# Kernel optimization log

Measured on AMD Instinct MI355X. Metric: run time of the kernel, lower is better.

## Reference

```python
import jax, jax.numpy as jnp
import numpy as np

B, S, D, H = 4, 2048, 1024, 16
DH = D // H


def setup_inputs() -> dict:
    key = jax.random.key(0)
    ks = jax.random.split(key, 10)
    scale = 1.0 / np.sqrt(D)
    return {
        "query": jax.random.normal(ks[0], (B, S, D), dtype=jnp.float32),
        "mask": jax.random.randint(ks[1], (B, S, S), 0, 2).astype(jnp.bool_),
        "Wq": jax.random.normal(ks[2], (D, D), dtype=jnp.float32) * scale,
        "bq": jax.random.normal(ks[3], (D,), dtype=jnp.float32) * 0.01,
        "Wk": jax.random.normal(ks[4], (D, D), dtype=jnp.float32) * scale,
        "bk": jax.random.normal(ks[5], (D,), dtype=jnp.float32) * 0.01,
        "Wv": jax.random.normal(ks[6], (D, D), dtype=jnp.float32) * scale,
        "bv": jax.random.normal(ks[7], (D,), dtype=jnp.float32) * 0.01,
        "Wo": jax.random.normal(ks[8], (D, D), dtype=jnp.float32) * scale,
        "bo": jax.random.normal(ks[9], (D,), dtype=jnp.float32) * 0.01,
    }


def reference(query, mask, Wq, bq, Wk, bk, Wv, bv, Wo, bo):
    # Self-attention path (key=value=None): q,k,v all from `query`.
    # Linear layers use torch convention: x @ W.T + b.  [B,S,D]
    q = query @ Wq.T + bq
    k = query @ Wk.T + bk
    v = query @ Wv.T + bv

    # split heads: [B,S,D] -> [B,H,S,DH]
    def split(x):
        return x.reshape(B, S, H, DH).transpose(0, 2, 1, 3)

    q, k, v = split(q), split(k), split(v)

    # scaled dot-product scores: [B,H,Sq,Sk]
    scores = jnp.einsum("bhqd,bhkd->bhqk", q, k) / jnp.sqrt(
        jnp.asarray(DH, dtype=q.dtype)
    )
    # MULTIPLICATIVE mask (True where masked), broadcast over heads
    scores = scores * mask[:, None, :, :].astype(scores.dtype)

    attn = jax.nn.softmax(scores, axis=-1)  # [B,H,Sq,Sk]
    out = jnp.einsum("bhqk,bhkd->bhqd", attn, v)  # [B,H,Sq,DH]

    # merge heads: [B,H,S,DH] -> [B,S,D]
    out = out.transpose(0, 2, 1, 3).reshape(B, S, D)
    return out @ Wo.T + bo
```

## Files before the change

### kernel.cpp

```cpp
#include <hip/hip_runtime.h>
#include <hip/hip_bf16.h>

#define DEVINL __device__ __forceinline__

typedef __attribute__((ext_vector_type(8))) short bf16x8;
typedef __attribute__((ext_vector_type(4))) float f32x4;

static constexpr int Bb = 4, Ss = 2048, Dd = 1024, Hh = 16, DHh = 64;
#define QPRESCALE 0.18033688f

DEVINL unsigned short f2bf(float f) {
  union { float f; unsigned int u; } a; a.f = f;
  unsigned int u = a.u;
  return (unsigned short)((u + 0x7fffu + ((u >> 16) & 1u)) >> 16);
}

DEVINL unsigned short f2bf_rne(float f) {
  __hip_bfloat16 h = __float2bfloat16(f);
  return *reinterpret_cast<unsigned short*>(&h);
}

DEVINL float fexp2(float x) {
#if __has_builtin(__builtin_amdgcn_exp2f)
  return __builtin_amdgcn_exp2f(x);
#else
  float r; asm("v_exp_f32 %0, %1" : "=v"(r) : "v"(x)); return r;
#endif
}

DEVINL unsigned cvtpk_bf16(float lo, float hi) {
  unsigned r; asm("v_cvt_pk_bf16_f32 %0, %1, %2" : "=v"(r) : "v"(lo), "v"(hi));
  return r;
}

DEVINL void gload16(const void* g, void* l) {
  __builtin_amdgcn_global_load_lds((const __attribute__((address_space(1))) void*)g,
                                   (__attribute__((address_space(3))) void*)l, 16, 0, 0);
}

__global__ void cvt_f32_bf16(const float4* __restrict__ src, ushort* __restrict__ dst, int n4) {
  int i = blockIdx.x * blockDim.x + threadIdx.x;
  int stride = gridDim.x * blockDim.x;
  for (; i < n4; i += stride) {
    float4 v = src[i];
    ushort4 o;
    o.x = f2bf(v.x); o.y = f2bf(v.y); o.z = f2bf(v.z); o.w = f2bf(v.w);
    *reinterpret_cast<ushort4*>(dst + (size_t)i * 4) = o;
  }
}

__global__ void bias_cat(const float* __restrict__ bq, const float* __restrict__ bk,
                         const float* __restrict__ bv, float* __restrict__ bcat) {
  int i = blockIdx.x * blockDim.x + threadIdx.x;
  if (i < 1024) bcat[i] = bq[i];
  else if (i < 2048) bcat[i] = bk[i - 1024];
  else if (i < 3072) bcat[i] = bv[i - 2048];
}

__global__ void mask_bits(const int* __restrict__ mask, unsigned long long* __restrict__ bm) {
  const int tid = threadIdx.x, lane = tid & 63;
  const int gw = blockIdx.x * 4 + (tid >> 6);
  const int b = gw >> 16;
  const int rem = gw & 65535;
  const int s = rem >> 5, ch = rem & 31;
  int m = mask[((size_t)b * Ss + s) * Ss + ch * 64 + lane];
  unsigned long long bits = __ballot(m != 0);
  if (lane == 0) bm[((size_t)b * 32 + ch) * Ss + s] = bits;
}

template<int OUT_BF16, int QSCALE>
__global__ __launch_bounds__(256)
void gemm_bt(const ushort* __restrict__ A, const ushort* __restrict__ Bm,
             const float* __restrict__ bias, void* __restrict__ Cout,
             ushort* __restrict__ vT, int M, int N, int K, int ldc) {
  __shared__ short lA[128 * 32];
  __shared__ short lB[128 * 32];
  const int tid = threadIdx.x;
  const int lane = tid & 63;
  const int wid = tid >> 6;
  const int wm = wid >> 1, wn = wid & 1;
  const int row0 = blockIdx.x * 128, col0 = blockIdx.y * 128;
  const int lr = lane & 15, lk8 = (lane >> 4) * 8;

  f32x4 acc[4][4];
#pragma unroll
  for (int i = 0; i < 4; i++)
#pragma unroll
    for (int j = 0; j < 4; j++) acc[i][j] = (f32x4){0.f, 0.f, 0.f, 0.f};

  const int c0 = tid, c1 = tid + 256;
  const int r0s = c0 >> 2, k0s = c0 & 3;
  const int r1s = c1 >> 2, k1s = c1 & 3;

  for (int kk = 0; kk < K; kk += 32) {
    __syncthreads();
    gload16(A + (size_t)(row0 + r0s) * K + kk + k0s * 8, lA + c0 * 8);
    gload16(A + (size_t)(row0 + r1s) * K + kk + k1s * 8, lA + c1 * 8);
    gload16(Bm + (size_t)(col0 + r0s) * K + kk + k0s * 8, lB + c0 * 8);
    gload16(Bm + (size_t)(col0 + r1s) * K + kk + k1s * 8, lB + c1 * 8);
    __syncthreads();

    bf16x8 af[4], bfr[4];
#pragma unroll
    for (int i = 0; i < 4; i++)
      af[i] = *reinterpret_cast<const bf16x8*>(&lA[(wm * 64 + i * 16 + lr) * 32 + lk8]);
#pragma unroll
    for (int j = 0; j < 4; j++)
      bfr[j] = *reinterpret_cast<const bf16x8*>(&lB[(wn * 64 + j * 16 + lr) * 32 + lk8]);
#pragma unroll
    for (int i = 0; i < 4; i++)
#pragma unroll
      for (int j = 0; j < 4; j++)
        acc[i][j] = __builtin_amdgcn_mfma_f32_16x16x32_bf16(af[i], bfr[j], acc[i][j], 0, 0, 0);
  }

  if (QSCALE && col0 >= 2048) {
#pragma unroll
    for (int j = 0; j < 4; j++) {
      const int c = col0 + wn * 64 + j * 16 + lr;
      const float bv = bias[c];
      const int d = c - 2048;
#pragma unroll
      for (int i = 0; i < 4; i++) {
        const int rbase = row0 + wm * 64 + i * 16 + (lane >> 4) * 4;
        ushort4 o;
        o.x = f2bf_rne(acc[i][j][0] + bv);
        o.y = f2bf_rne(acc[i][j][1] + bv);
        o.z = f2bf_rne(acc[i][j][2] + bv);
        o.w = f2bf_rne(acc[i][j][3] + bv);
        *reinterpret_cast<ushort4*>(&vT[(size_t)d * 8192 + rbase]) = o;
      }
    }
  } else {
#pragma unroll
    for (int j = 0; j < 4; j++) {
      const int c = col0 + wn * 64 + j * 16 + lr;
      const float bv = bias[c];
      const float qs = (QSCALE && c < 1024) ? QPRESCALE : 1.0f;
#pragma unroll
      for (int i = 0; i < 4; i++) {
        const int rbase = row0 + wm * 64 + i * 16 + (lane >> 4) * 4;
#pragma unroll
        for (int t = 0; t < 4; t++) {
          float v = (acc[i][j][t] + bv) * qs;
          if (OUT_BF16)
            reinterpret_cast<ushort*>(Cout)[(size_t)(rbase + t) * ldc + c] = f2bf_rne(v);
          else
            reinterpret_cast<float*>(Cout)[(size_t)(rbase + t) * ldc + c] = v;
        }
      }
    }
  }
}

__global__ __launch_bounds__(256)
void attn_fwd(const ushort* __restrict__ qkv, const ushort* __restrict__ vT,
              const unsigned long long* __restrict__ bmask, ushort* __restrict__ ctx) {
  const int qt = blockIdx.x, h = blockIdx.y, b = blockIdx.z;
  const int tid = threadIdx.x, lane = tid & 63, wid = tid >> 6;
  const int q0 = qt * 64;
  const int lr = lane & 15, lg = lane >> 4;
  const int RS = 2048;

  __shared__ short lK[64 * 64];
  __shared__ short lVt[64 * 64];

  const size_t rowb = (size_t)b * Ss;
  const ushort* Kg = qkv + rowb * RS + 1024 + h * 64;
  const ushort* Vtg = vT + (size_t)(h * 64) * 8192 + b * 2048;
  const unsigned long long* Mg = bmask + (size_t)b * 32 * Ss + q0 + wid * 16 + lr;

  const int kn0 = tid, kn1 = tid + 256;
  const int r0 = kn0 >> 3, p0 = kn0 & 7;
  const int r1 = kn1 >> 3, p1 = kn1 & 7;
  const int sg0 = (r0 & 3) | (((r0 >> 3) & 1) << 2);
  const int sg1 = (r1 & 3) | (((r1 >> 3) & 1) << 2);
  const int k_c0 = (p0 ^ sg0) * 8, k_c1 = (p1 ^ sg1) * 8;
  const int v_c0 = (p0 ^ (r0 & 7)) * 8, v_c1 = (p1 ^ (r1 & 7)) * 8;

  bf16x8 qf[2];
  {
    const ushort* gq = qkv + (rowb + q0 + wid * 16 + lr) * RS + h * 64;
    qf[0] = *reinterpret_cast<const bf16x8*>(gq + lg * 8);
    qf[1] = *reinterpret_cast<const bf16x8*>(gq + 32 + lg * 8);
  }

  f32x4 oacc[4];
#pragma unroll
  for (int j = 0; j < 4; j++) oacc[j] = (f32x4){0.f, 0.f, 0.f, 0.f};
  float lp = 0.f;

  const int s0 = (lg ^ (lr & 7)) * 8;
  const int Rbase = ((lr >> 2) << 3) + (lr & 3);

  for (int t = 0; t < Ss / 64; ++t) {
    __syncthreads();
    gload16(Kg + ((size_t)t * 64 + r0) * RS + k_c0, lK + kn0 * 8);
    gload16(Kg + ((size_t)t * 64 + r1) * RS + k_c1, lK + kn1 * 8);
    gload16(Vtg + (size_t)r0 * 8192 + t * 64 + v_c0, lVt + kn0 * 8);
    gload16(Vtg + (size_t)r1 * 8192 + t * 64 + v_c1, lVt + kn1 * 8);
    const unsigned long long m64 = Mg[(size_t)t * Ss];
    __syncthreads();

    f32x4 sc[4];
    __builtin_amdgcn_s_setprio(1);
#pragma unroll
    for (int f = 0; f < 4; ++f) {
      const int R = Rbase + ((f & 1) << 2) + ((f >> 1) << 5);
      bf16x8 kb0 = *reinterpret_cast<const bf16x8*>(&lK[R * 64 + s0]);
      bf16x8 kb1 = *reinterpret_cast<const bf16x8*>(&lK[R * 64 + (s0 ^ 32)]);
      f32x4 z = (f32x4){0.f, 0.f, 0.f, 0.f};
      z = __builtin_amdgcn_mfma_f32_16x16x32_bf16(kb0, qf[0], z, 0, 0, 0);
      z = __builtin_amdgcn_mfma_f32_16x16x32_bf16(kb1, qf[1], z, 0, 0, 0);
      sc[f] = z;
    }
    __builtin_amdgcn_s_setprio(0);

    const unsigned blo = (unsigned)(m64 >> (lg * 8));
    const unsigned bhi = (unsigned)(m64 >> (32 + lg * 8));
#pragma unroll
    for (int f = 0; f < 4; ++f) {
      const unsigned bits = (f >= 2) ? bhi : blo;
#pragma unroll
      for (int r = 0; r < 4; ++r) {
        const int pos = ((f & 1) << 2) + r;
        const int keep = ((int)(bits << (31 - pos))) >> 31;
        float ps = __int_as_float(__float_as_int(sc[f][r]) & keep);
        float pe = fexp2(ps);
        sc[f][r] = pe;
        lp += pe;
      }
    }

    union VU { unsigned u[4]; bf16x8 v; } ua, ub;
    ua.u[0] = cvtpk_bf16(sc[0][0], sc[0][1]);
    ua.u[1] = cvtpk_bf16(sc[0][2], sc[0][3]);
    ua.u[2] = cvtpk_bf16(sc[1][0], sc[1][1]);
    ua.u[3] = cvtpk_bf16(sc[1][2], sc[1][3]);
    ub.u[0] = cvtpk_bf16(sc[2][0], sc[2][1]);
    ub.u[1] = cvtpk_bf16(sc[2][2], sc[2][3]);
    ub.u[2] = cvtpk_bf16(sc[3][0], sc[3][1]);
    ub.u[3] = cvtpk_bf16(sc[3][2], sc[3][3]);

    __builtin_amdgcn_s_setprio(1);
#pragma unroll
    for (int j = 0; j < 4; ++j) {
      const int row = j * 16 + lr;
      bf16x8 vb0 = *reinterpret_cast<const bf16x8*>(&lVt[row * 64 + s0]);
      bf16x8 vb1 = *reinterpret_cast<const bf16x8*>(&lVt[row * 64 + (s0 ^ 32)]);
      oacc[j] = __builtin_amdgcn_mfma_f32_16x16x32_bf16(ua.v, vb0, oacc[j], 0, 0, 0);
      oacc[j] = __builtin_amdgcn_mfma_f32_16x16x32_bf16(ub.v, vb1, oacc[j], 0, 0, 0);
    }
    __builtin_amdgcn_s_setprio(0);
  }

  lp += __shfl_xor(lp, 16, 64);
  lp += __shfl_xor(lp, 32, 64);
  const float inv = 1.0f / lp;
  float invr[4];
#pragma unroll
  for (int r = 0; r < 4; ++r) invr[r] = __shfl(inv, 4 * lg + r, 64);
#pragma unroll
  for (int j = 0; j < 4; j++)
#pragma unroll
    for (int r = 0; r < 4; r++) {
      const int row = q0 + wid * 16 + 4 * lg + r;
      const int col = h * DHh + j * 16 + lr;
      ctx[(rowb + row) * Dd + col] = (short)f2bf_rne(oacc[j][r] * invr[r]);
    }
}

extern "C" void kernel_launch(void* const* d_in, const int* in_sizes, int n_in,
                              void* d_out, int out_size, void* d_ws, size_t ws_size,
                              hipStream_t stream) {
  const float* query = (const float*)d_in[0];
  const int* mask = (const int*)d_in[1];
  const float* Wq = (const float*)d_in[2];
  const float* bq = (const float*)d_in[3];
  const float* Wk = (const float*)d_in[4];
  const float* bk = (const float*)d_in[5];
  const float* Wv = (const float*)d_in[6];
  const float* bv = (const float*)d_in[7];
  const float* Wo = (const float*)d_in[8];
  const float* bo = (const float*)d_in[9];
  float* out = (float*)d_out;

  ushort* ws = (ushort*)d_ws;
  const size_t SZ_X = (size_t)8192 * 1024;
  ushort* xB   = ws;
  ushort* ctx  = ws;
  ushort* qkvB = ws + SZ_X;
  ushort* wcat = qkvB + (size_t)8192 * 2048;
  ushort* woB  = wcat + (size_t)3072 * 1024;
  float*  bcat = (float*)(woB + (size_t)1024 * 1024);
  unsigned long long* bmask = (unsigned long long*)((char*)bcat + 16384);
  ushort* vT   = (ushort*)((char*)bmask + (size_t)2 * 1024 * 1024);

  dim3 blk(256);
  cvt_f32_bf16<<<2048, blk, 0, stream>>>((const float4*)query, xB, (int)(SZ_X / 4));
  cvt_f32_bf16<<<512, blk, 0, stream>>>((const float4*)Wq, wcat, 1024 * 1024 / 4);
  cvt_f32_bf16<<<512, blk, 0, stream>>>((const float4*)Wk, wcat + 1048576, 1024 * 1024 / 4);
  cvt_f32_bf16<<<512, blk, 0, stream>>>((const float4*)Wv, wcat + 2097152, 1024 * 1024 / 4);
  cvt_f32_bf16<<<512, blk, 0, stream>>>((const float4*)Wo, woB, 1024 * 1024 / 4);
  bias_cat<<<12, blk, 0, stream>>>(bq, bk, bv, bcat);
  mask_bits<<<65536, blk, 0, stream>>>(mask, bmask);

  dim3 gqkv(64, 24);
  gemm_bt<1, 1><<<gqkv, blk, 0, stream>>>(xB, wcat, bcat, qkvB, vT, 8192, 3072, 1024, 2048);

  dim3 ga(32, 16, 4);
  attn_fwd<<<ga, blk, 0, stream>>>(qkvB, vT, bmask, ctx);

  dim3 go(64, 8);
  gemm_bt<0, 0><<<go, blk, 0, stream>>>(ctx, woB, bo, out, nullptr, 8192, 1024, 1024, 1024);
}
```

Measured before the change: 396.9 us.

## Merge input conversions into one prep kernel and move V transpose to a separate pass

The five f32-to-bf16 conversion launches and the bias concat are merged into a single grid-stride prep kernel, which cuts launch overhead. The QKV GEMM epilogue no longer writes V transposed with scattered strided stores. It now writes V row-major into a widened 3072-column buffer, and a new LDS-based vtrans kernel produces the transposed V with coalesced writes. This adds one extra read and write pass over V in exchange for coalesced GEMM stores.

Result: no change. 391.9 us (-1.2%).

```diff
diff --git a/kernel.cpp b/kernel.cpp
--- a/kernel.cpp
+++ b/kernel.cpp
@@ -38,23 +38,30 @@
                                    (__attribute__((address_space(3))) void*)l, 16, 0, 0);
 }
 
-__global__ void cvt_f32_bf16(const float4* __restrict__ src, ushort* __restrict__ dst, int n4) {
-  int i = blockIdx.x * blockDim.x + threadIdx.x;
-  int stride = gridDim.x * blockDim.x;
-  for (; i < n4; i += stride) {
-    float4 v = src[i];
-    ushort4 o;
-    o.x = f2bf(v.x); o.y = f2bf(v.y); o.z = f2bf(v.z); o.w = f2bf(v.w);
-    *reinterpret_cast<ushort4*>(dst + (size_t)i * 4) = o;
-  }
-}
-
-__global__ void bias_cat(const float* __restrict__ bq, const float* __restrict__ bk,
-                         const float* __restrict__ bv, float* __restrict__ bcat) {
-  int i = blockIdx.x * blockDim.x + threadIdx.x;
-  if (i < 1024) bcat[i] = bq[i];
-  else if (i < 2048) bcat[i] = bk[i - 1024];
-  else if (i < 3072) bcat[i] = bv[i - 2048];
+DEVINL void cvt4(float4 v, ushort* dst) {
+  ushort4 o;
+  o.x = f2bf(v.x); o.y = f2bf(v.y); o.z = f2bf(v.z); o.w = f2bf(v.w);
+  *reinterpret_cast<ushort4*>(dst) = o;
+}
+
+__global__ void prep(const float4* __restrict__ query,
+                     const float4* __restrict__ Wq, const float4* __restrict__ Wk,
+                     const float4* __restrict__ Wv, const float4* __restrict__ Wo,
+                     const float* __restrict__ bq, const float* __restrict__ bk,
+                     const float* __restrict__ bv,
+                     ushort* __restrict__ xB, ushort* __restrict__ wcat,
+                     ushort* __restrict__ woB, float* __restrict__ bcat) {
+  const int i = blockIdx.x * blockDim.x + threadIdx.x;
+  const int stride = gridDim.x * blockDim.x;
+  for (int t = i; t < 2097152; t += stride) cvt4(query[t], xB + (size_t)t * 4);
+  for (int t = i; t < 262144; t += stride) {
+    cvt4(Wq[t], wcat + (size_t)t * 4);
+    cvt4(Wk[t], wcat + 1048576 + (size_t)t * 4);
+    cvt4(Wv[t], wcat + 2097152 + (size_t)t * 4);
+    cvt4(Wo[t], woB + (size_t)t * 4);
+  }
+  for (int t = i; t < 3072; t += stride)
+    bcat[t] = (t < 1024) ? bq[t] : (t < 2048) ? bk[t - 1024] : bv[t - 2048];
 }
 
 __global__ void mask_bits(const int* __restrict__ mask, unsigned long long* __restrict__ bm) {
@@ -72,7 +79,7 @@
 __global__ __launch_bounds__(256)
 void gemm_bt(const ushort* __restrict__ A, const ushort* __restrict__ Bm,
              const float* __restrict__ bias, void* __restrict__ Cout,
-             ushort* __restrict__ vT, int M, int N, int K, int ldc) {
+             int M, int N, int K, int ldc) {
   __shared__ short lA[128 * 32];
   __shared__ short lB[128 * 32];
   const int tid = threadIdx.x;
@@ -114,42 +121,48 @@
         acc[i][j] = __builtin_amdgcn_mfma_f32_16x16x32_bf16(af[i], bfr[j], acc[i][j], 0, 0, 0);
   }
 
-  if (QSCALE && col0 >= 2048) {
-#pragma unroll
-    for (int j = 0; j < 4; j++) {
-      const int c = col0 + wn * 64 + j * 16 + lr;
-      const float bv = bias[c];
-      const int d = c - 2048;
-#pragma unroll
-      for (int i = 0; i < 4; i++) {
-        const int rbase = row0 + wm * 64 + i * 16 + (lane >> 4) * 4;
-        ushort4 o;
-        o.x = f2bf_rne(acc[i][j][0] + bv);
-        o.y = f2bf_rne(acc[i][j][1] + bv);
-        o.z = f2bf_rne(acc[i][j][2] + bv);
-        o.w = f2bf_rne(acc[i][j][3] + bv);
-        *reinterpret_cast<ushort4*>(&vT[(size_t)d * 8192 + rbase]) = o;
+#pragma unroll
+  for (int j = 0; j < 4; j++) {
+    const int c = col0 + wn * 64 + j * 16 + lr;
+    const float bv = bias[c];
+    const float qs = (QSCALE && c < 1024) ? QPRESCALE : 1.0f;
+#pragma unroll
+    for (int i = 0; i < 4; i++) {
+      const int rbase = row0 + wm * 64 + i * 16 + (lane >> 4) * 4;
+#pragma unroll
+      for (int t = 0; t < 4; t++) {
+        float v = (acc[i][j][t] + bv) * qs;
+        if (OUT_BF16)
+          reinterpret_cast<ushort*>(Cout)[(size_t)(rbase + t) * ldc + c] = f2bf_rne(v);
+        else
+          reinterpret_cast<float*>(Cout)[(size_t)(rbase + t) * ldc + c] = v;
       }
     }
-  } else {
-#pragma unroll
-    for (int j = 0; j < 4; j++) {
-      const int c = col0 + wn * 64 + j * 16 + lr;
-      const float bv = bias[c];
-      const float qs = (QSCALE && c < 1024) ? QPRESCALE : 1.0f;
-#pragma unroll
-      for (int i = 0; i < 4; i++) {
-        const int rbase = row0 + wm * 64 + i * 16 + (lane >> 4) * 4;
-#pragma unroll
-        for (int t = 0; t < 4; t++) {
-          float v = (acc[i][j][t] + bv) * qs;
-          if (OUT_BF16)
-            reinterpret_cast<ushort*>(Cout)[(size_t)(rbase + t) * ldc + c] = f2bf_rne(v);
-          else
-            reinterpret_cast<float*>(Cout)[(size_t)(rbase + t) * ldc + c] = v;
-        }
-      }
-    }
+  }
+}
+
+__global__ __launch_bounds__(256)
+void vtrans(const ushort* __restrict__ qkv, ushort* __restrict__ vT) {
+  __shared__ short lT[64 * 66];
+  const int g0 = blockIdx.x * 64, d0 = blockIdx.y * 64;
+  const int tid = threadIdx.x;
+#pragma unroll
+  for (int half = 0; half < 2; half++) {
+    const int row = (tid >> 3) + half * 32;
+    const int seg = tid & 7;
+    bf16x8 v = *reinterpret_cast<const bf16x8*>(
+        qkv + (size_t)(g0 + row) * 3072 + 2048 + d0 + seg * 8);
+#pragma unroll
+    for (int e = 0; e < 8; e++) lT[(seg * 8 + e) * 66 + row] = v[e];
+  }
+  __syncthreads();
+  {
+    const int d = tid >> 2, sg = tid & 3;
+    bf16x8 a = *reinterpret_cast<const bf16x8*>(&lT[d * 66 + sg * 16]);
+    bf16x8 b = *reinterpret_cast<const bf16x8*>(&lT[d * 66 + sg * 16 + 8]);
+    ushort* dst = vT + (size_t)(d0 + d) * 8192 + g0 + sg * 16;
+    *reinterpret_cast<bf16x8*>(dst) = a;
+    *reinterpret_cast<bf16x8*>(dst + 8) = b;
   }
 }
 
@@ -160,7 +173,7 @@
   const int tid = threadIdx.x, lane = tid & 63, wid = tid >> 6;
   const int q0 = qt * 64;
   const int lr = lane & 15, lg = lane >> 4;
-  const int RS = 2048;
+  const int RS = 3072;
 
   __shared__ short lK[64 * 64];
   __shared__ short lVt[64 * 64];
@@ -290,27 +303,27 @@
   ushort* xB   = ws;
   ushort* ctx  = ws;
   ushort* qkvB = ws + SZ_X;
-  ushort* wcat = qkvB + (size_t)8192 * 2048;
+  ushort* wcat = qkvB + (size_t)8192 * 3072;
   ushort* woB  = wcat + (size_t)3072 * 1024;
   float*  bcat = (float*)(woB + (size_t)1024 * 1024);
   unsigned long long* bmask = (unsigned long long*)((char*)bcat + 16384);
   ushort* vT   = (ushort*)((char*)bmask + (size_t)2 * 1024 * 1024);
 
   dim3 blk(256);
-  cvt_f32_bf16<<<2048, blk, 0, stream>>>((const float4*)query, xB, (int)(SZ_X / 4));
-  cvt_f32_bf16<<<512, blk, 0, stream>>>((const float4*)Wq, wcat, 1024 * 1024 / 4);
-  cvt_f32_bf16<<<512, blk, 0, stream>>>((const float4*)Wk, wcat + 1048576, 1024 * 1024 / 4);
-  cvt_f32_bf16<<<512, blk, 0, stream>>>((const float4*)Wv, wcat + 2097152, 1024 * 1024 / 4);
-  cvt_f32_bf16<<<512, blk, 0, stream>>>((const float4*)Wo, woB, 1024 * 1024 / 4);
-  bias_cat<<<12, blk, 0, stream>>>(bq, bk, bv, bcat);
+  prep<<<2048, blk, 0, stream>>>((const float4*)query, (const float4*)Wq,
+                                 (const float4*)Wk, (const float4*)Wv, (const float4*)Wo,
+                                 bq, bk, bv, xB, wcat, woB, bcat);
   mask_bits<<<65536, blk, 0, stream>>>(mask, bmask);
 
   dim3 gqkv(64, 24);
-  gemm_bt<1, 1><<<gqkv, blk, 0, stream>>>(xB, wcat, bcat, qkvB, vT, 8192, 3072, 1024, 2048);
+  gemm_bt<1, 1><<<gqkv, blk, 0, stream>>>(xB, wcat, bcat, qkvB, 8192, 3072, 1024, 3072);
+
+  dim3 gvt(128, 16);
+  vtrans<<<gvt, blk, 0, stream>>>(qkvB, vT);
 
   dim3 ga(32, 16, 4);
   attn_fwd<<<ga, blk, 0, stream>>>(qkvB, vT, bmask, ctx);
 
   dim3 go(64, 8);
-  gemm_bt<0, 0><<<go, blk, 0, stream>>>(ctx, woB, bo, out, nullptr, 8192, 1024, 1024, 1024);
-}
+  gemm_bt<0, 0><<<go, blk, 0, stream>>>(ctx, woB, bo, out, 8192, 1024, 1024, 1024);
+}
```
